# Kernel optimization log

Hardware: AMD Instinct MI355X
Metric: run time of the kernel (lower is better)

Reference implementation:

```python
import jax, jax.numpy as jnp
import numpy as np

N, L, D = 64, 510, 768
L1, K, OUT = 128, 20, 300
EPS = 1e-5


def _make_spans(key, n, n_spans, max_len):
    ks, kl = jax.random.split(key)
    starts = jnp.sort(jax.random.randint(ks, (n, n_spans), 0, max_len - 4), axis=1)
    lens = jax.random.randint(kl, (n, n_spans), 1, 5)
    ends = jnp.minimum(starts + lens, max_len)
    return starts.astype(jnp.int32), ends.astype(jnp.int32)


def setup_inputs() -> dict:
    key = jax.random.key(0)
    ks = jax.random.split(key, 10)
    t1 = jax.random.normal(ks[0], (N, L, D), jnp.float32)
    encoded_know = jax.random.normal(ks[1], (N, L, D), jnp.float32)
    span_starts, span_ends = _make_spans(ks[2], N, L1, L)
    know_span_starts, know_span_ends = _make_spans(ks[3], N, K, L)
    # padding masks: True = masked; guarantee >=1 valid entry per row
    valid1 = jax.random.randint(ks[4], (N,), L1 // 2, L1 + 1)
    key_padding_mask = jnp.arange(L1)[None, :] >= valid1[:, None]
    validk = jax.random.randint(ks[5], (N,), 5, K + 1)
    key_padding_mask_know = jnp.arange(K)[None, :] >= validk[:, None]
    W_lin = jax.random.normal(ks[6], (OUT, D), jnp.float32) * 0.02
    b_lin = jnp.zeros((OUT,), jnp.float32)
    gamma = jnp.ones((OUT,), jnp.float32)
    beta = jnp.zeros((OUT,), jnp.float32)
    W_score = jax.random.normal(ks[7], (1, OUT), jnp.float32) * 0.02
    b_score = jnp.zeros((1,), jnp.float32)
    return dict(t1=t1, encoded_know=encoded_know,
                span_starts=span_starts, span_ends=span_ends,
                key_padding_mask=key_padding_mask,
                know_span_starts=know_span_starts, know_span_ends=know_span_ends,
                key_padding_mask_know=key_padding_mask_know,
                W_lin=W_lin, b_lin=b_lin, gamma=gamma, beta=beta,
                W_score=W_score, b_score=b_score)


def _span_mean(x, starts, ends):
    # x: (N,L,D); spans [s,e) -> mean via inclusive-scan difference (one pass)
    n, l, d = x.shape
    cs = jnp.concatenate([jnp.zeros((n, 1, d), x.dtype), jnp.cumsum(x, axis=1)], axis=1)
    gather = lambda idx: jnp.take_along_axis(cs, idx[:, :, None].astype(jnp.int32), axis=1)
    sums = gather(ends) - gather(starts)  # (N, n_spans, D)
    lens = jnp.maximum(ends - starts, 1).astype(x.dtype)[:, :, None]
    return sums / lens


def _layernorm(x, g, b):
    m = jnp.mean(x, axis=-1, keepdims=True)
    v = jnp.mean(jnp.square(x - m), axis=-1, keepdims=True)
    return (x - m) * jax.lax.rsqrt(v + EPS) * g + b


def reference(t1, encoded_know, span_starts, span_ends, key_padding_mask,
              know_span_starts, know_span_ends, key_padding_mask_know,
              W_lin, b_lin, gamma, beta, W_score, b_score):
    lam = 1.0

    def branch(x, s, e, mask):
        pooled = _span_mean(x, s, e)                       # ragged segment mean
        h = _layernorm(pooled @ W_lin.T + b_lin, gamma, beta)
        sc = (h @ W_score.T + b_score)[..., 0]             # (N, n_spans)
        sc = jnp.where(mask, -jnp.inf, sc)                 # masked_fill
        return h, jax.nn.softmax(sc * lam, axis=1)

    h1, s1 = branch(t1, span_starts, span_ends, key_padding_mask)
    hk, sk = branch(encoded_know, know_span_starts, know_span_ends, key_padding_mask_know)
    score = jnp.broadcast_to(s1[:, :, None], h1.shape)     # repeat to (N,L1,OUT)
    return h1, score, hk, sk
```

## Files before the change

kernel.cpp:

```cpp
#include <hip/hip_runtime.h>
#include <hip/hip_bf16.h>
#include <stdint.h>

#define NB    64
#define LSEQ  510
#define DIN   768
#define L1S   128
#define KS    20
#define OUTF  300
#define NPAD  320
#define EPSL  1e-5f

#define M1    (NB * L1S)
#define MK    (NB * KS)
#define MT    (M1 + MK)

#define OFF_H1    0
#define OFF_SCORE (M1 * OUTF)
#define OFF_HK    (2 * M1 * OUTF)
#define OFF_SK    (OFF_HK + MK * OUTF)

#define WS_FLAG    0
#define WS_SCORES  64
#define WS_WBF     81920

typedef short  short8_t  __attribute__((ext_vector_type(8)));
typedef float  float4v_t __attribute__((ext_vector_type(4)));
typedef unsigned short ushort4_t __attribute__((ext_vector_type(4)));

#define SA_STRIDE 776
#define SC_STRIDE 324
#define LDS_BYTES 41984

__device__ inline bool mask_at(const void* m, int idx, int flag) {
    switch (flag) {
        case 1:  return ((const unsigned char*)m)[idx] != 0;
        case 2:  return ((const float*)m)[idx] != 0.0f;
        case 3:  return ((const unsigned short*)m)[idx] != 0;
        default: return ((const int*)m)[idx] != 0;
    }
}

__global__ __launch_bounds__(256)
void prep_kernel(const unsigned int* __restrict__ p, int* __restrict__ flag,
                 const float* __restrict__ W, unsigned short* __restrict__ Wb) {
    if (blockIdx.x == 0) {
        __shared__ int f_bf16, f_f32, f_other;
        if (threadIdx.x == 0) { f_bf16 = 0; f_f32 = 0; f_other = 0; }
        __syncthreads();
        for (int i = threadIdx.x; i < 2048; i += blockDim.x) {
            unsigned int v = p[i];
            if (v <= 1u) continue;
            if (v == 0x3F803F80u)       atomicOr(&f_bf16, 1);
            else if (v == 0x3F800000u)  atomicOr(&f_f32, 1);
            else                        atomicOr(&f_other, 1);
        }
        __syncthreads();
        if (threadIdx.x == 0) {
            int f = 0;
            if (f_bf16)       f = 3;
            else if (f_f32)   f = 2;
            else if (f_other) f = 1;
            *flag = f;
        }
        return;
    }
    int idx = (blockIdx.x - 1) * 256 + threadIdx.x;
    if (idx >= NPAD * DIN) return;
    int r = idx / DIN;
    float v = (r < OUTF) ? W[idx] : 0.f;
    __hip_bfloat16 b = __float2bfloat16(v);
    Wb[idx] = *(unsigned short*)&b;
}

__global__ __launch_bounds__(640, 5)
void fused_gemm_kernel(const float* __restrict__ t1,
                       const float* __restrict__ know,
                       const int* __restrict__ s1s, const int* __restrict__ s1e,
                       const int* __restrict__ kss, const int* __restrict__ kse,
                       const unsigned short* __restrict__ Wb,
                       const float* __restrict__ bias,
                       const float* __restrict__ gamma,
                       const float* __restrict__ beta,
                       const float* __restrict__ Wsc,
                       const float* __restrict__ bsc,
                       float* __restrict__ out,
                       float* __restrict__ scores) {
    __shared__ unsigned long long lds_raw[LDS_BYTES / 8];
    unsigned short* sA   = (unsigned short*)lds_raw;
    int*   sSrc = (int*)  ((char*)lds_raw + 16 * 1552);
    int*   sLen = (int*)  ((char*)lds_raw + 16 * 1552 + 64);
    float* sInv = (float*)((char*)lds_raw + 16 * 1552 + 128);

    const int tid = threadIdx.x;
    const int R0  = blockIdx.x * 16;
    const bool isk = (R0 >= M1);

    if (tid < 16) {
        int g = R0 + tid;
        int s, e, n;
        if (!isk) { n = g >> 7;          s = s1s[g];      e = s1e[g]; }
        else      { int gg = g - M1; n = gg / KS; s = kss[gg]; e = kse[gg]; }
        if (s < 0) s = 0;
        if (e > LSEQ) e = LSEQ;
        int len = e - s; if (len < 1) len = 1;
        sSrc[tid] = n * (LSEQ * (DIN / 4)) + s * (DIN / 4);
        sLen[tid] = len;
        sInv[tid] = 1.0f / (float)len;
    }
    __syncthreads();

    const float4* src4 = (const float4*)(isk ? know : t1);
    for (int t = tid; t < 16 * 192; t += 640) {
        int sp = t / 192;
        int c4 = t - sp * 192;
        const float4* p = src4 + sSrc[sp] + c4;
        int len = sLen[sp];
        float4 acc = p[0];
        for (int r = 1; r < len; ++r) {
            float4 v = p[r * 192];
            acc.x += v.x; acc.y += v.y; acc.z += v.z; acc.w += v.w;
        }
        float inv = sInv[sp];
        __hip_bfloat16 b0 = __float2bfloat16(acc.x * inv);
        __hip_bfloat16 b1 = __float2bfloat16(acc.y * inv);
        __hip_bfloat16 b2 = __float2bfloat16(acc.z * inv);
        __hip_bfloat16 b3 = __float2bfloat16(acc.w * inv);
        ushort4_t pk;
        pk.x = *(unsigned short*)&b0; pk.y = *(unsigned short*)&b1;
        pk.z = *(unsigned short*)&b2; pk.w = *(unsigned short*)&b3;
        *(ushort4_t*)(sA + sp * SA_STRIDE + c4 * 4) = pk;
    }
    __syncthreads();

    const int wave = tid >> 6;
    const int lane = tid & 63;
    const int quad = lane >> 4;
    const int l16  = lane & 15;
    const int cg   = wave % 5;
    const int kh   = wave / 5;

    const unsigned short* sArow = sA + l16 * SA_STRIDE + quad * 8 + kh * 384;
    const unsigned short* bb = Wb + (size_t)(cg * 64 + l16) * DIN + quad * 8 + kh * 384;

    float4v_t acc0 = {0.f, 0.f, 0.f, 0.f};
    float4v_t acc1 = {0.f, 0.f, 0.f, 0.f};
    float4v_t acc2 = {0.f, 0.f, 0.f, 0.f};
    float4v_t acc3 = {0.f, 0.f, 0.f, 0.f};

#pragma unroll 4
    for (int k0 = 0; k0 < 384; k0 += 32) {
        short8_t a  = *(const short8_t*)(sArow + k0);
        short8_t b0 = *(const short8_t*)(bb + 0 * 16 * DIN + k0);
        short8_t b1 = *(const short8_t*)(bb + 1 * 16 * DIN + k0);
        short8_t b2 = *(const short8_t*)(bb + 2 * 16 * DIN + k0);
        short8_t b3 = *(const short8_t*)(bb + 3 * 16 * DIN + k0);
        acc0 = __builtin_amdgcn_mfma_f32_16x16x32_bf16(a, b0, acc0, 0, 0, 0);
        acc1 = __builtin_amdgcn_mfma_f32_16x16x32_bf16(a, b1, acc1, 0, 0, 0);
        acc2 = __builtin_amdgcn_mfma_f32_16x16x32_bf16(a, b2, acc2, 0, 0, 0);
        acc3 = __builtin_amdgcn_mfma_f32_16x16x32_bf16(a, b3, acc3, 0, 0, 0);
    }

    __syncthreads();
    float* sC = (float*)lds_raw;
#pragma unroll
    for (int i = 0; i < 4; ++i) {
        int r = (kh * 16 + quad * 4 + i) * SC_STRIDE + cg * 64 + l16;
        sC[r +  0] = acc0[i];
        sC[r + 16] = acc1[i];
        sC[r + 32] = acc2[i];
        sC[r + 48] = acc3[i];
    }
    __syncthreads();

    if (wave < 8) {
        const float bs0 = bsc[0];
#pragma unroll
        for (int rr = 0; rr < 2; ++rr) {
            const int r = wave * 2 + rr;
            const int g = R0 + r;
            float tv[5];
            float s = 0.f;
#pragma unroll
            for (int m = 0; m < 5; ++m) {
                int c = lane + 64 * m;
                float v = 0.f;
                if (c < OUTF)
                    v = sC[r * SC_STRIDE + c] + sC[(16 + r) * SC_STRIDE + c] + bias[c];
                tv[m] = v; s += v;
            }
#pragma unroll
            for (int off = 32; off > 0; off >>= 1) s += __shfl_xor(s, off, 64);
            const float mean = s * (1.0f / OUTF);
            float vs = 0.f;
#pragma unroll
            for (int m = 0; m < 5; ++m) {
                int c = lane + 64 * m;
                float d = (c < OUTF) ? (tv[m] - mean) : 0.f;
                vs += d * d;
            }
#pragma unroll
            for (int off = 32; off > 0; off >>= 1) vs += __shfl_xor(vs, off, 64);
            const float rstd = rsqrtf(vs * (1.0f / OUTF) + EPSL);

            const size_t off0 = isk ? (size_t)OFF_HK + (size_t)(g - M1) * OUTF
                                    : (size_t)g * OUTF;
            float sc = 0.f;
#pragma unroll
            for (int m = 0; m < 5; ++m) {
                int c = lane + 64 * m;
                if (c < OUTF) {
                    float h = (tv[m] - mean) * rstd * gamma[c] + beta[c];
                    out[off0 + c] = h;
                    sc += h * Wsc[c];
                }
            }
#pragma unroll
            for (int off = 32; off > 0; off >>= 1) sc += __shfl_xor(sc, off, 64);
            if (lane == 0) scores[g] = sc + bs0;
        }
    }
}

__global__ __launch_bounds__(128)
void softmax_bcast_kernel(const float* __restrict__ scores,
                          const void* __restrict__ m1,
                          const void* __restrict__ mk,
                          const int* __restrict__ flagp,
                          float* __restrict__ out) {
    const int flag = *flagp;
    const int b = blockIdx.x;
    const int tid = threadIdx.x;
    const int lane = tid & 63;

    if (b < NB * 5) {
        __shared__ float sprob[L1S];
        const int n = b / 5;
        const int chunk = b - n * 5;
        if (tid < 64) {
            float v0 = scores[n * L1S + lane];
            float v1 = scores[n * L1S + lane + 64];
            if (mask_at(m1, n * L1S + lane, flag))      v0 = -INFINITY;
            if (mask_at(m1, n * L1S + lane + 64, flag)) v1 = -INFINITY;
            float mx = fmaxf(v0, v1);
#pragma unroll
            for (int off = 32; off > 0; off >>= 1) mx = fmaxf(mx, __shfl_xor(mx, off, 64));
            float e0 = __expf(v0 - mx);
            float e1 = __expf(v1 - mx);
            float s = e0 + e1;
#pragma unroll
            for (int off = 32; off > 0; off >>= 1) s += __shfl_xor(s, off, 64);
            float inv = 1.0f / s;
            sprob[lane]      = e0 * inv;
            sprob[lane + 64] = e1 * inv;
        }
        __syncthreads();
        float* dst = out + (size_t)OFF_SCORE + (size_t)n * (L1S * OUTF);
        const int cbase = chunk * 7680;
#pragma unroll
        for (int i = 0; i < 15; ++i) {
            int e0i = cbase + (i * 128 + tid) * 4;
            float4 v;
            v.x = sprob[(e0i + 0) / OUTF];
            v.y = sprob[(e0i + 1) / OUTF];
            v.z = sprob[(e0i + 2) / OUTF];
            v.w = sprob[(e0i + 3) / OUTF];
            *(float4*)(dst + e0i) = v;
        }
    } else {
        const int n = (b - NB * 5) * 2 + (tid >> 6);
        float v = -INFINITY;
        if (lane < KS) {
            v = scores[M1 + n * KS + lane];
            if (mask_at(mk, n * KS + lane, flag)) v = -INFINITY;
        }
        float mx = v;
#pragma unroll
        for (int off = 32; off > 0; off >>= 1) mx = fmaxf(mx, __shfl_xor(mx, off, 64));
        float e = (lane < KS) ? __expf(v - mx) : 0.f;
        float s = e;
#pragma unroll
        for (int off = 32; off > 0; off >>= 1) s += __shfl_xor(s, off, 64);
        if (lane < KS) out[(size_t)OFF_SK + n * KS + lane] = e / s;
    }
}

extern "C" void kernel_launch(void* const* d_in, const int* in_sizes, int n_in,
                              void* d_out, int out_size, void* d_ws, size_t ws_size,
                              hipStream_t stream) {
    const float* t1   = (const float*)d_in[0];
    const float* know = (const float*)d_in[1];
    const int* s1s = (const int*)d_in[2];
    const int* s1e = (const int*)d_in[3];
    const void* m1 = d_in[4];
    const int* kss = (const int*)d_in[5];
    const int* kse = (const int*)d_in[6];
    const void* mk = d_in[7];
    const float* Wl  = (const float*)d_in[8];
    const float* bl  = (const float*)d_in[9];
    const float* gm  = (const float*)d_in[10];
    const float* bt  = (const float*)d_in[11];
    const float* Wsc = (const float*)d_in[12];
    const float* bsc = (const float*)d_in[13];
    float* out = (float*)d_out;

    char* ws = (char*)d_ws;
    int*            flag   = (int*)(ws + WS_FLAG);
    float*          scores = (float*)(ws + WS_SCORES);
    unsigned short* Wb     = (unsigned short*)(ws + WS_WBF);

    prep_kernel<<<1 + (NPAD * DIN + 255) / 256, 256, 0, stream>>>(
        (const unsigned int*)m1, flag, Wl, Wb);
    fused_gemm_kernel<<<MT / 16, 640, 0, stream>>>(t1, know, s1s, s1e, kss, kse,
                                                   Wb, bl, gm, bt, Wsc, bsc,
                                                   out, scores);
    softmax_bcast_kernel<<<NB * 5 + NB / 2, 128, 0, stream>>>(scores, m1, mk,
                                                              flag, out);
}
```

Before: 264.5 us.

## Drop split-K and LDS epilogue; fuse LayerNorm stats in registers via cross-wave reductions

The GEMM is restructured so each of the 10 waves owns 32 output columns over the full K=768, instead of 5 column groups times 2 K-halves. This removes the partial-sum staging tile in LDS. LayerNorm mean and variance and the score dot product are now computed directly from the MFMA accumulators, using lane shuffles plus a small cross-wave reduction in shared memory. The variance uses the E[x^2]-mean^2 form. Together these shrink LDS use and raise the occupancy hint from 5 to 8, at the cost of a longer serial K loop per wave, slightly less precise variance, and out-of-range column waves doing wasted MFMA work.

```diff
diff --git a/kernel.cpp b/kernel.cpp
--- a/kernel.cpp
+++ b/kernel.cpp
@@ -29,8 +29,6 @@
 typedef unsigned short ushort4_t __attribute__((ext_vector_type(4)));
 
 #define SA_STRIDE 776
-#define SC_STRIDE 324
-#define LDS_BYTES 41984
 
 __device__ inline bool mask_at(const void* m, int idx, int flag) {
     switch (flag) {
@@ -73,7 +71,7 @@
     Wb[idx] = *(unsigned short*)&b;
 }
 
-__global__ __launch_bounds__(640, 5)
+__global__ __launch_bounds__(640, 8)
 void fused_gemm_kernel(const float* __restrict__ t1,
                        const float* __restrict__ know,
                        const int* __restrict__ s1s, const int* __restrict__ s1e,
@@ -86,11 +84,13 @@
                        const float* __restrict__ bsc,
                        float* __restrict__ out,
                        float* __restrict__ scores) {
-    __shared__ unsigned long long lds_raw[LDS_BYTES / 8];
-    unsigned short* sA   = (unsigned short*)lds_raw;
-    int*   sSrc = (int*)  ((char*)lds_raw + 16 * 1552);
-    int*   sLen = (int*)  ((char*)lds_raw + 16 * 1552 + 64);
-    float* sInv = (float*)((char*)lds_raw + 16 * 1552 + 128);
+    __shared__ unsigned short sA[16 * SA_STRIDE];
+    __shared__ int   sSrc[16];
+    __shared__ int   sLen[16];
+    __shared__ float sInv[16];
+    __shared__ float sSum[10][16];
+    __shared__ float sSq[10][16];
+    __shared__ float sScore[10][16];
 
     const int tid = threadIdx.x;
     const int R0  = blockIdx.x * 16;
@@ -137,87 +137,109 @@
     const int lane = tid & 63;
     const int quad = lane >> 4;
     const int l16  = lane & 15;
-    const int cg   = wave % 5;
-    const int kh   = wave / 5;
-
-    const unsigned short* sArow = sA + l16 * SA_STRIDE + quad * 8 + kh * 384;
-    const unsigned short* bb = Wb + (size_t)(cg * 64 + l16) * DIN + quad * 8 + kh * 384;
+
+    const unsigned short* sArow = sA + l16 * SA_STRIDE + quad * 8;
+    const unsigned short* bb0 = Wb + (size_t)(wave * 32 + l16) * DIN + quad * 8;
+    const unsigned short* bb1 = bb0 + 16 * DIN;
 
     float4v_t acc0 = {0.f, 0.f, 0.f, 0.f};
     float4v_t acc1 = {0.f, 0.f, 0.f, 0.f};
-    float4v_t acc2 = {0.f, 0.f, 0.f, 0.f};
-    float4v_t acc3 = {0.f, 0.f, 0.f, 0.f};
 
 #pragma unroll 4
-    for (int k0 = 0; k0 < 384; k0 += 32) {
+    for (int k0 = 0; k0 < DIN; k0 += 32) {
         short8_t a  = *(const short8_t*)(sArow + k0);
-        short8_t b0 = *(const short8_t*)(bb + 0 * 16 * DIN + k0);
-        short8_t b1 = *(const short8_t*)(bb + 1 * 16 * DIN + k0);
-        short8_t b2 = *(const short8_t*)(bb + 2 * 16 * DIN + k0);
-        short8_t b3 = *(const short8_t*)(bb + 3 * 16 * DIN + k0);
+        short8_t b0 = *(const short8_t*)(bb0 + k0);
+        short8_t b1 = *(const short8_t*)(bb1 + k0);
         acc0 = __builtin_amdgcn_mfma_f32_16x16x32_bf16(a, b0, acc0, 0, 0, 0);
         acc1 = __builtin_amdgcn_mfma_f32_16x16x32_bf16(a, b1, acc1, 0, 0, 0);
-        acc2 = __builtin_amdgcn_mfma_f32_16x16x32_bf16(a, b2, acc2, 0, 0, 0);
-        acc3 = __builtin_amdgcn_mfma_f32_16x16x32_bf16(a, b3, acc3, 0, 0, 0);
-    }
-
+    }
+
+    const int c0 = wave * 32 + l16;
+    const int c1 = c0 + 16;
+    const bool v0 = (c0 < OUTF);
+    const bool v1 = (c1 < OUTF);
+    const float bias0 = v0 ? bias[c0]  : 0.f;
+    const float bias1 = v1 ? bias[c1]  : 0.f;
+    const float gam0  = v0 ? gamma[c0] : 0.f;
+    const float gam1  = v1 ? gamma[c1] : 0.f;
+    const float bet0  = v0 ? beta[c0]  : 0.f;
+    const float bet1  = v1 ? beta[c1]  : 0.f;
+    const float wsc0  = v0 ? Wsc[c0]   : 0.f;
+    const float wsc1  = v1 ? Wsc[c1]   : 0.f;
+
+    float x0[4], x1[4], rs[4], rq[4];
+#pragma unroll
+    for (int i = 0; i < 4; ++i) {
+        x0[i] = v0 ? acc0[i] + bias0 : 0.f;
+        x1[i] = v1 ? acc1[i] + bias1 : 0.f;
+        rs[i] = x0[i] + x1[i];
+        rq[i] = x0[i] * x0[i] + x1[i] * x1[i];
+    }
+#pragma unroll
+    for (int off = 1; off <= 8; off <<= 1) {
+#pragma unroll
+        for (int i = 0; i < 4; ++i) {
+            rs[i] += __shfl_xor(rs[i], off, 64);
+            rq[i] += __shfl_xor(rq[i], off, 64);
+        }
+    }
+    if (l16 == 0) {
+#pragma unroll
+        for (int i = 0; i < 4; ++i) {
+            sSum[wave][quad * 4 + i] = rs[i];
+            sSq[wave][quad * 4 + i]  = rq[i];
+        }
+    }
     __syncthreads();
-    float* sC = (float*)lds_raw;
+
+    float mean[4], rstd[4];
 #pragma unroll
     for (int i = 0; i < 4; ++i) {
-        int r = (kh * 16 + quad * 4 + i) * SC_STRIDE + cg * 64 + l16;
-        sC[r +  0] = acc0[i];
-        sC[r + 16] = acc1[i];
-        sC[r + 32] = acc2[i];
-        sC[r + 48] = acc3[i];
+        float ts = 0.f, tq = 0.f;
+#pragma unroll
+        for (int w2 = 0; w2 < 10; ++w2) {
+            ts += sSum[w2][quad * 4 + i];
+            tq += sSq[w2][quad * 4 + i];
+        }
+        float m = ts * (1.0f / OUTF);
+        mean[i] = m;
+        rstd[i] = rsqrtf(tq * (1.0f / OUTF) - m * m + EPSL);
+    }
+
+    float scp[4];
+#pragma unroll
+    for (int i = 0; i < 4; ++i) {
+        const int row = quad * 4 + i;
+        const int g = R0 + row;
+        const size_t off0 = isk ? (size_t)OFF_HK + (size_t)(g - M1) * OUTF
+                                : (size_t)g * OUTF;
+        float sc = 0.f;
+        if (v0) { float h = (x0[i] - mean[i]) * rstd[i] * gam0 + bet0;
+                  out[off0 + c0] = h; sc += h * wsc0; }
+        if (v1) { float h = (x1[i] - mean[i]) * rstd[i] * gam1 + bet1;
+                  out[off0 + c1] = h; sc += h * wsc1; }
+        scp[i] = sc;
+    }
+#pragma unroll
+    for (int off = 1; off <= 8; off <<= 1) {
+#pragma unroll
+        for (int i = 0; i < 4; ++i) scp[i] += __shfl_xor(scp[i], off, 64);
+    }
+    if (l16 == 0) {
+#pragma unroll
+        for (int i = 0; i < 4; ++i) sScore[wave][quad * 4 + i] = scp[i];
     }
     __syncthreads();
 
-    if (wave < 8) {
+    if (wave == 0 && l16 == 0) {
         const float bs0 = bsc[0];
 #pragma unroll
-        for (int rr = 0; rr < 2; ++rr) {
-            const int r = wave * 2 + rr;
-            const int g = R0 + r;
-            float tv[5];
-            float s = 0.f;
-#pragma unroll
-            for (int m = 0; m < 5; ++m) {
-                int c = lane + 64 * m;
-                float v = 0.f;
-                if (c < OUTF)
-                    v = sC[r * SC_STRIDE + c] + sC[(16 + r) * SC_STRIDE + c] + bias[c];
-                tv[m] = v; s += v;
-            }
-#pragma unroll
-            for (int off = 32; off > 0; off >>= 1) s += __shfl_xor(s, off, 64);
-            const float mean = s * (1.0f / OUTF);
-            float vs = 0.f;
-#pragma unroll
-            for (int m = 0; m < 5; ++m) {
-                int c = lane + 64 * m;
-                float d = (c < OUTF) ? (tv[m] - mean) : 0.f;
-                vs += d * d;
-            }
-#pragma unroll
-            for (int off = 32; off > 0; off >>= 1) vs += __shfl_xor(vs, off, 64);
-            const float rstd = rsqrtf(vs * (1.0f / OUTF) + EPSL);
-
-            const size_t off0 = isk ? (size_t)OFF_HK + (size_t)(g - M1) * OUTF
-                                    : (size_t)g * OUTF;
-            float sc = 0.f;
-#pragma unroll
-            for (int m = 0; m < 5; ++m) {
-                int c = lane + 64 * m;
-                if (c < OUTF) {
-                    float h = (tv[m] - mean) * rstd * gamma[c] + beta[c];
-                    out[off0 + c] = h;
-                    sc += h * Wsc[c];
-                }
-            }
-#pragma unroll
-            for (int off = 32; off > 0; off >>= 1) sc += __shfl_xor(sc, off, 64);
-            if (lane == 0) scores[g] = sc + bs0;
+        for (int i = 0; i < 4; ++i) {
+            const int row = quad * 4 + i;
+            float ss = 0.f;
+#pragma unroll
+            for (int w2 = 0; w2 < 10; ++w2) ss += sScore[w2][row];
+            scores[R0 + row] = ss + bs0;
         }
     }
 }
```

Result: slower. 296.8 us (+12.2%).
